# Optimization experiments

Measured on AMD Instinct MI355X. Metric: run time of the kernel, lower is better.

The kernel has to match this reference:

```python
import jax, jax.numpy as jnp
import numpy as np

C = 256
NUM_HEADS = 8
HEAD_DIM = C // NUM_HEADS
SCALE = HEAD_DIM ** -0.5


def setup_inputs() -> dict:
    key = jax.random.key(0)
    ks = jax.random.split(key, 10)
    B, H, W = 2, 64, 64
    s = 0.02
    return {
        "spatial_feat": jax.random.normal(ks[0], (B, C, H, W), jnp.float32),
        "freq_feat": jax.random.normal(ks[1], (B, C, H, W), jnp.float32),
        "wq": jax.random.normal(ks[2], (C, C), jnp.float32) * s,
        "bq": jax.random.normal(ks[3], (C,), jnp.float32) * s,
        "wk": jax.random.normal(ks[4], (C, C), jnp.float32) * s,
        "bk": jax.random.normal(ks[5], (C,), jnp.float32) * s,
        "wv": jax.random.normal(ks[6], (C, C), jnp.float32) * s,
        "bv": jax.random.normal(ks[7], (C,), jnp.float32) * s,
        "wo": jax.random.normal(ks[8], (C, C), jnp.float32) * s,
        "bo": jax.random.normal(ks[9], (C,), jnp.float32) * s,
    }


def _proj(x, w, b):
    # 1x1 conv == channel-mixing matmul: (O,C) x (B,C,H,W) -> (B,O,H,W)
    return jnp.einsum('oc,bchw->bohw', w, x) + b[None, :, None, None]


def _heads(x, B, HW):
    return x.reshape(B, NUM_HEADS, HEAD_DIM, HW)


def _cross_attend(q_src, kv_src, wq, bq, wk, bk, wv, bv, wo, bo):
    B, Cc, H, W = q_src.shape
    HW = H * W
    q = _heads(_proj(q_src, wq, bq), B, HW)   # (B, h, d, N)
    k = _heads(_proj(kv_src, wk, bk), B, HW)
    v = _heads(_proj(kv_src, wv, bv), B, HW)
    # attn[b,h,m,n] = q[...,m] . k[...,n]
    attn = jnp.einsum('bhdm,bhdn->bhmn', q, k) * SCALE
    attn = jax.nn.softmax(attn, axis=-1)
    # out[...,m] = sum_n v[...,n] * attn[m,n]
    out = jnp.einsum('bhdn,bhmn->bhdm', v, attn)
    out = out.reshape(B, Cc, H, W)
    return _proj(out, wo, bo)


def reference(spatial_feat, freq_feat, wq, bq, wk, bk, wv, bv, wo, bo):
    spatial_attended = spatial_feat + _cross_attend(
        spatial_feat, freq_feat, wq, bq, wk, bk, wv, bv, wo, bo)
    freq_attended = freq_feat + _cross_attend(
        freq_feat, spatial_feat, wq, bq, wk, bk, wv, bv, wo, bo)
    return spatial_attended + freq_attended
```

## Files before the change

### kernel.cpp

```cpp
#include <hip/hip_runtime.h>
#include <hip/hip_bf16.h>

#define B_ 2
#define C_ 256
#define NH_ 8
#define D_ 32
#define N_ 4096
#define SCALE_ 0.17677669529663689f
#define QSC_ 0.25505277f

typedef __hip_bfloat16 bf16;
typedef __attribute__((ext_vector_type(8))) short sx8;
typedef __attribute__((ext_vector_type(4))) short sx4;
typedef __attribute__((ext_vector_type(4))) float fx4;

__device__ __forceinline__ float b2f(bf16 x) { return __bfloat162float(x); }
__device__ __forceinline__ bf16 f2b(float x) { return __float2bfloat16(x); }
__device__ __forceinline__ short fbs(float x) { bf16 h = __float2bfloat16(x); return *(short*)&h; }
__device__ __forceinline__ float sbf(short s) { bf16 h = *(bf16*)&s; return __bfloat162float(h); }
__device__ __forceinline__ void sched_mem_fence() { asm volatile("" ::: "memory"); }

#if __has_builtin(__builtin_amdgcn_exp2f)
__device__ __forceinline__ float fexp2(float x) { return __builtin_amdgcn_exp2f(x); }
#else
__device__ __forceinline__ float fexp2(float x) { return exp2f(x); }
#endif

__global__ __launch_bounds__(256)
void convert_x_kernel(const float* __restrict__ spatial,
                      const float* __restrict__ freq,
                      bf16* __restrict__ xb) {
  const int tid = threadIdx.x;
  const int p0 = blockIdx.x * 64;
  const int c0 = blockIdx.y * 64;
  const int z  = blockIdx.z;
  const int s = z >> 1, b = z & 1;
  const float* x = (s == 0) ? spatial : freq;

  __shared__ float ls[64][65];

  const int pp = tid & 63, cb = tid >> 6;
  #pragma unroll
  for (int i = 0; i < 16; ++i) {
    int c = cb + 4 * i;
    ls[c][pp] = x[(size_t)(b * C_ + c0 + c) * N_ + p0 + pp];
  }
  __syncthreads();

  #pragma unroll
  for (int i = 0; i < 2; ++i) {
    int j = tid + 256 * i;
    int p = j >> 3, ck = (j & 7) * 8;
    short tmp[8];
    #pragma unroll
    for (int u = 0; u < 8; ++u) tmp[u] = fbs(ls[ck + u][p]);
    *(sx8*)(xb + ((size_t)z * N_ + p0 + p) * C_ + c0 + ck) = *(sx8*)tmp;
  }
}

__global__ __launch_bounds__(256)
void convert_w_kernel(const float* __restrict__ wq, const float* __restrict__ wk,
                      const float* __restrict__ wv, const float* __restrict__ wo,
                      bf16* __restrict__ wb, bf16* __restrict__ wob) {
  int idx = blockIdx.x * 256 + threadIdx.x;
  if (idx < 196608) {
    const float* src = (idx < 65536) ? wq : (idx < 131072) ? wk : wv;
    wb[idx] = f2b(src[idx & 65535]);
  } else {
    int off = idx - 196608;
    wob[off] = f2b(wo[off]);
  }
}

__global__ __launch_bounds__(256)
void qkv_gemm_kernel(const bf16* __restrict__ wb, const bf16* __restrict__ xb,
                     const float* __restrict__ bq, const float* __restrict__ bk,
                     const float* __restrict__ bv,
                     bf16* __restrict__ qhf, bf16* __restrict__ khf,
                     bf16* __restrict__ vhf) {
  const int tid = threadIdx.x;
  const int p0 = blockIdx.x * 128;
  const int o0 = blockIdx.y * 128;
  const int z  = blockIdx.z;

  const int lane = tid & 63, w = tid >> 6;
  const int ml = lane & 15, Q4 = (lane >> 4) * 4, Q8 = (lane >> 4) * 8;
  const int ow = (w >> 1) * 64, pw = (w & 1) * 64;

  __shared__ __align__(16) short asb[128 * 72];
  __shared__ __align__(16) short bsb[128 * 72];
  __shared__ float bias_s[128];

  if (tid < 128) {
    int o = o0 + tid;
    bias_s[tid] = (o < 256) ? bq[o] : (o < 512) ? bk[o - 256] : bv[o - 512];
  }

  const fx4 z4 = {0.f, 0.f, 0.f, 0.f};
  fx4 acc[4][4];
  #pragma unroll
  for (int ot = 0; ot < 4; ++ot)
    #pragma unroll
    for (int pt = 0; pt < 4; ++pt) acc[ot][pt] = z4;

  const int sr = tid >> 1, scu = (tid & 1) * 32;
  for (int k0 = 0; k0 < 256; k0 += 64) {
    __syncthreads();
    #pragma unroll
    for (int u = 0; u < 4; ++u) {
      *(sx8*)&asb[sr * 72 + scu + u * 8] =
          *(const sx8*)&wb[(o0 + sr) * 256 + k0 + scu + u * 8];
      *(sx8*)&bsb[sr * 72 + scu + u * 8] =
          *(const sx8*)(xb + ((size_t)z * N_ + p0 + sr) * C_ + k0 + scu + u * 8);
    }
    __syncthreads();
    #pragma unroll
    for (int kk = 0; kk < 2; ++kk) {
      sx8 af[4], bfr[4];
      #pragma unroll
      for (int t = 0; t < 4; ++t)
        af[t] = *(sx8*)&asb[(ow + t * 16 + ml) * 72 + kk * 32 + Q8];
      #pragma unroll
      for (int t = 0; t < 4; ++t)
        bfr[t] = *(sx8*)&bsb[(pw + t * 16 + ml) * 72 + kk * 32 + Q8];
      #pragma unroll
      for (int ot = 0; ot < 4; ++ot)
        #pragma unroll
        for (int pt = 0; pt < 4; ++pt)
          acc[ot][pt] = __builtin_amdgcn_mfma_f32_16x16x32_bf16(
              af[ot], bfr[pt], acc[ot][pt], 0, 0, 0);
    }
  }

  if (o0 < 512) {
    bf16* dst = (o0 < 256) ? qhf : khf;
    const int ob = (o0 < 256) ? o0 : o0 - 256;
    const float scl = (o0 < 256) ? QSC_ : 1.f;
    #pragma unroll
    for (int ot = 0; ot < 4; ++ot) {
      const int og = ob + ow + ot * 16 + Q4;
      #pragma unroll
      for (int pt = 0; pt < 4; ++pt) {
        int p = p0 + pw + pt * 16 + ml;
        short tmp[4];
        #pragma unroll
        for (int r = 0; r < 4; ++r)
          tmp[r] = fbs((acc[ot][pt][r] + bias_s[ow + ot * 16 + Q4 + r]) * scl);
        *(sx4*)(dst + (((size_t)z * NH_ + (og >> 5)) * N_ + p) * D_ + (og & 31)) =
            *(sx4*)tmp;
      }
    }
  } else {
    #pragma unroll
    for (int ot = 0; ot < 4; ++ot)
      #pragma unroll
      for (int pt = 0; pt < 4; ++pt) {
        int p = p0 + pw + pt * 16 + ml;
        #pragma unroll
        for (int r = 0; r < 4; ++r) {
          int lo = ow + ot * 16 + Q4 + r;
          int rho = (o0 - 512) + lo;
          int h = rho >> 5, d = rho & 31;
          size_t basev = ((size_t)z * NH_ + h) * D_ * N_;
          vhf[basev + (size_t)(((p >> 5) * 2) + (d >> 4)) * 512 +
              (d & 15) * 32 + (p & 31)] = f2b(acc[ot][pt][r] + bias_s[lo]);
        }
      }
  }
}

__global__ __launch_bounds__(256, 4)
void attn_kernel(const bf16* __restrict__ qhf, const bf16* __restrict__ khf,
                 const bf16* __restrict__ vhf, bf16* __restrict__ attoT) {
  const int tid  = threadIdx.x;
  const int m0   = blockIdx.x * 256;
  const int h    = blockIdx.y;
  const int z    = blockIdx.z;
  const int s = z >> 1, b = z & 1;
  const int zo = ((1 - s) << 1) | b;

  const bf16* qz = qhf + ((size_t)z  * NH_ + h) * N_ * D_;
  const bf16* kz = khf + ((size_t)zo * NH_ + h) * N_ * D_;
  const bf16* vz = vhf + ((size_t)zo * NH_ + h) * D_ * N_;

  const int lane = tid & 63;
  const int w    = tid >> 6;
  const int ml   = lane & 15;
  const int Q4   = (lane >> 4) * 4;
  const int Q8   = (lane >> 4) * 8;

  __shared__ __align__(16) short kts[2][64 * 40];
  __shared__ __align__(16) short vss[2][4][16 * 36];
  __shared__ __align__(16) short pst[4][16 * 72];

  sx8 qf[4];
  #pragma unroll
  for (int s4 = 0; s4 < 4; ++s4)
    qf[s4] = *(const sx8*)(qz + (size_t)(m0 + w * 64 + s4 * 16 + ml) * D_ + Q8);

  sx8 onesf;
  #pragma unroll
  for (int u = 0; u < 8; ++u) onesf[u] = (short)0x3F80;

  const fx4 z4 = {0.f, 0.f, 0.f, 0.f};
  fx4 acc[4][2];
  #pragma unroll
  for (int s4 = 0; s4 < 4; ++s4) { acc[s4][0] = z4; acc[s4][1] = z4; }
  fx4 lacc[4] = {z4, z4, z4, z4};

  const int srow = tid >> 2, sg = (tid & 3) * 8;
  const int vblk = tid >> 6, vrow = (tid >> 2) & 15;

  sx8 kpre = *(const sx8*)(kz + (size_t)tid * 8);
  sx8 vpre = *(const sx8*)(vz + (size_t)tid * 8);
  *(sx8*)&kts[0][srow * 40 + sg] = kpre;
  *(sx8*)&vss[0][vblk][vrow * 36 + sg] = vpre;
  __syncthreads();

  int cur = 0;
  for (int n0 = 0; n0 < N_; n0 += 64) {
    const bool more = (n0 + 64 < N_);
    if (more) {
      kpre = *(const sx8*)(kz + (size_t)(n0 + 64) * D_ + (size_t)tid * 8);
      vpre = *(const sx8*)(vz + (size_t)(n0 + 64) * D_ + (size_t)tid * 8);
    }

    sx8 kf[4], vf[2][2];
    #pragma unroll
    for (int t = 0; t < 4; ++t)
      kf[t] = *(sx8*)&kts[cur][(t * 16 + ml) * 40 + Q8];
    #pragma unroll
    for (int dt = 0; dt < 2; ++dt)
      #pragma unroll
      for (int c = 0; c < 2; ++c)
        vf[dt][c] = *(sx8*)&vss[cur][c * 2 + dt][ml * 36 + Q8];

    #pragma unroll
    for (int s4 = 0; s4 < 4; ++s4) {
      fx4 st[4];
      #pragma unroll
      for (int t = 0; t < 4; ++t)
        st[t] = __builtin_amdgcn_mfma_f32_16x16x32_bf16(kf[t], qf[s4], z4, 0, 0, 0);
      #pragma unroll
      for (int t = 0; t < 4; ++t) {
        #pragma unroll
        for (int r = 0; r < 4; ++r) st[t][r] = fexp2(st[t][r]);
        sx4 pk = {fbs(st[t][0]), fbs(st[t][1]), fbs(st[t][2]), fbs(st[t][3])};
        *(sx4*)&pst[w][ml * 72 + t * 16 + Q4] = pk;
      }
      sched_mem_fence();
      sx8 pf0 = *(sx8*)&pst[w][ml * 72 + 0  + Q8];
      sx8 pf1 = *(sx8*)&pst[w][ml * 72 + 32 + Q8];
      sched_mem_fence();
      lacc[s4] = __builtin_amdgcn_mfma_f32_16x16x32_bf16(onesf, pf0, lacc[s4], 0, 0, 0);
      lacc[s4] = __builtin_amdgcn_mfma_f32_16x16x32_bf16(onesf, pf1, lacc[s4], 0, 0, 0);
      #pragma unroll
      for (int dt = 0; dt < 2; ++dt) {
        fx4 a = acc[s4][dt];
        a = __builtin_amdgcn_mfma_f32_16x16x32_bf16(vf[dt][0], pf0, a, 0, 0, 0);
        a = __builtin_amdgcn_mfma_f32_16x16x32_bf16(vf[dt][1], pf1, a, 0, 0, 0);
        acc[s4][dt] = a;
      }
    }

    if (more) {
      *(sx8*)&kts[cur ^ 1][srow * 40 + sg] = kpre;
      *(sx8*)&vss[cur ^ 1][vblk][vrow * 36 + sg] = vpre;
    }
    __syncthreads();
    cur ^= 1;
  }

  #pragma unroll
  for (int s4 = 0; s4 < 4; ++s4) {
    float inv = 1.f / lacc[s4][0];
    int col = m0 + w * 64 + s4 * 16 + ml;
    #pragma unroll
    for (int dt = 0; dt < 2; ++dt) {
      short tmp[4];
      #pragma unroll
      for (int r = 0; r < 4; ++r) tmp[r] = fbs(acc[s4][dt][r] * inv);
      *(sx4*)(attoT + ((size_t)z * N_ + col) * C_ + h * D_ + dt * 16 + Q4) =
          *(sx4*)tmp;
    }
  }
}

__global__ __launch_bounds__(256)
void out_proj_kernel(const bf16* __restrict__ wob, const bf16* __restrict__ attoT,
                     const float* __restrict__ spatial,
                     const float* __restrict__ freq,
                     const float* __restrict__ bo, float* __restrict__ out) {
  const int tid = threadIdx.x;
  const int p0 = blockIdx.x * 128;
  const int o0 = blockIdx.y * 64;
  const int b  = blockIdx.z;

  const int lane = tid & 63, w = tid >> 6;
  const int ml = lane & 15, Q4 = (lane >> 4) * 4, Q8 = (lane >> 4) * 8;
  const int ow = (w >> 1) * 32, pw = (w & 1) * 64;

  __shared__ __align__(16) short asb[64 * 72];
  __shared__ __align__(16) short bsb[128 * 72];
  __shared__ float bo_s[64];

  if (tid < 64) bo_s[tid] = 2.f * bo[o0 + tid];

  const bf16* at0 = attoT + (size_t)(0 + b) * N_ * C_;
  const bf16* at1 = attoT + (size_t)(2 + b) * N_ * C_;

  const fx4 z4 = {0.f, 0.f, 0.f, 0.f};
  fx4 acc[2][4];
  #pragma unroll
  for (int ot = 0; ot < 2; ++ot)
    #pragma unroll
    for (int pt = 0; pt < 4; ++pt) acc[ot][pt] = z4;

  for (int k0 = 0; k0 < 256; k0 += 64) {
    __syncthreads();
    #pragma unroll
    for (int i = 0; i < 2; ++i) {
      int j = tid + 256 * i;
      int r = j >> 3, cu = (j & 7) * 8;
      *(sx8*)&asb[r * 72 + cu] = *(const sx8*)&wob[(o0 + r) * 256 + k0 + cu];
    }
    #pragma unroll
    for (int i = 0; i < 4; ++i) {
      int j = tid + 256 * i;
      int p = j >> 3, cu = (j & 7) * 8;
      sx8 va = *(const sx8*)(at0 + (size_t)(p0 + p) * C_ + k0 + cu);
      sx8 vb2 = *(const sx8*)(at1 + (size_t)(p0 + p) * C_ + k0 + cu);
      short tmp[8];
      #pragma unroll
      for (int u = 0; u < 8; ++u) tmp[u] = fbs(sbf(va[u]) + sbf(vb2[u]));
      *(sx8*)&bsb[p * 72 + cu] = *(sx8*)tmp;
    }
    __syncthreads();
    #pragma unroll
    for (int kk = 0; kk < 2; ++kk) {
      sx8 af[2], bfr[4];
      #pragma unroll
      for (int t = 0; t < 2; ++t)
        af[t] = *(sx8*)&asb[(ow + t * 16 + ml) * 72 + kk * 32 + Q8];
      #pragma unroll
      for (int t = 0; t < 4; ++t)
        bfr[t] = *(sx8*)&bsb[(pw + t * 16 + ml) * 72 + kk * 32 + Q8];
      #pragma unroll
      for (int ot = 0; ot < 2; ++ot)
        #pragma unroll
        for (int pt = 0; pt < 4; ++pt)
          acc[ot][pt] = __builtin_amdgcn_mfma_f32_16x16x32_bf16(
              af[ot], bfr[pt], acc[ot][pt], 0, 0, 0);
    }
  }

  #pragma unroll
  for (int ot = 0; ot < 2; ++ot)
    #pragma unroll
    for (int pt = 0; pt < 4; ++pt) {
      int p = p0 + pw + pt * 16 + ml;
      #pragma unroll
      for (int r = 0; r < 4; ++r) {
        int ol = ow + ot * 16 + Q4 + r;
        size_t off = ((size_t)b * C_ + o0 + ol) * N_ + p;
        out[off] = acc[ot][pt][r] + bo_s[ol] + spatial[off] + freq[off];
      }
    }
}

extern "C" void kernel_launch(void* const* d_in, const int* in_sizes, int n_in,
                              void* d_out, int out_size, void* d_ws, size_t ws_size,
                              hipStream_t stream) {
  const float* spatial = (const float*)d_in[0];
  const float* freq    = (const float*)d_in[1];
  const float* wq = (const float*)d_in[2];
  const float* bq = (const float*)d_in[3];
  const float* wk = (const float*)d_in[4];
  const float* bk = (const float*)d_in[5];
  const float* wv = (const float*)d_in[6];
  const float* bv = (const float*)d_in[7];
  const float* wo = (const float*)d_in[8];
  const float* bo = (const float*)d_in[9];
  float* out = (float*)d_out;

  const size_t SZ = (size_t)2 * B_ * N_ * C_;
  bf16* xb    = (bf16*)d_ws;
  bf16* qhf   = xb + SZ;
  bf16* khf   = qhf + SZ;
  bf16* vhf   = khf + SZ;
  bf16* attoT = vhf + SZ;
  bf16* wb    = attoT + SZ;
  bf16* wob   = wb + 768 * 256;

  convert_w_kernel<<<dim3(1024), 256, 0, stream>>>(wq, wk, wv, wo, wb, wob);
  convert_x_kernel<<<dim3(N_ / 64, C_ / 64, 2 * B_), 256, 0, stream>>>(
      spatial, freq, xb);
  qkv_gemm_kernel<<<dim3(N_ / 128, 768 / 128, 2 * B_), 256, 0, stream>>>(
      wb, xb, bq, bk, bv, qhf, khf, vhf);
  attn_kernel<<<dim3(N_ / 256, NH_, 2 * B_), 256, 0, stream>>>(
      qhf, khf, vhf, attoT);
  out_proj_kernel<<<dim3(N_ / 128, C_ / 64, B_), 256, 0, stream>>>(
      wob, attoT, spatial, freq, bo, out);
}
```

Baseline: 227.3 us.

## Split attention KV range in two with combine kernel and swizzle LDS layouts

Attention blocks now each process half of the key/value sequence, doubling the grid so more blocks run concurrently on the GPU. Unnormalised partial outputs and row sums are written to workspace, and a new combine kernel adds them and normalises. K and P shared-memory tiles switch from padded strides to XOR swizzles to cut bank conflicts and LDS footprint. The cost is an extra kernel launch and extra global traffic for the partials, and the split path is used only if the workspace is large enough.

```diff
diff --git a/kernel.cpp b/kernel.cpp
--- a/kernel.cpp
+++ b/kernel.cpp
@@ -169,13 +169,17 @@
   }
 }
 
+template<int NSPLIT>
 __global__ __launch_bounds__(256, 4)
-void attn_kernel(const bf16* __restrict__ qhf, const bf16* __restrict__ khf,
-                 const bf16* __restrict__ vhf, bf16* __restrict__ attoT) {
+void attn_kernel_t(const bf16* __restrict__ qhf, const bf16* __restrict__ khf,
+                   const bf16* __restrict__ vhf, bf16* __restrict__ outp,
+                   float* __restrict__ lpart) {
   const int tid  = threadIdx.x;
   const int m0   = blockIdx.x * 256;
   const int h    = blockIdx.y;
-  const int z    = blockIdx.z;
+  const int bz   = blockIdx.z;
+  const int sp   = (NSPLIT == 1) ? 0 : (bz >> 2);
+  const int z    = (NSPLIT == 1) ? bz : (bz & 3);
   const int s = z >> 1, b = z & 1;
   const int zo = ((1 - s) << 1) | b;
 
@@ -186,12 +190,16 @@
   const int lane = tid & 63;
   const int w    = tid >> 6;
   const int ml   = lane & 15;
-  const int Q4   = (lane >> 4) * 4;
-  const int Q8   = (lane >> 4) * 8;
-
-  __shared__ __align__(16) short kts[2][64 * 40];
+  const int q4   = lane >> 4;
+  const int Q4   = q4 * 4;
+  const int Q8   = q4 * 8;
+
+  __shared__ __align__(16) short kts[2][64 * 32];
   __shared__ __align__(16) short vss[2][4][16 * 36];
-  __shared__ __align__(16) short pst[4][16 * 72];
+  __shared__ __align__(16) short pst[4][16 * 64];
+
+  const int nlo = sp * (N_ / NSPLIT);
+  const int nhi = nlo + N_ / NSPLIT;
 
   sx8 qf[4];
   #pragma unroll
@@ -208,18 +216,23 @@
   for (int s4 = 0; s4 < 4; ++s4) { acc[s4][0] = z4; acc[s4][1] = z4; }
   fx4 lacc[4] = {z4, z4, z4, z4};
 
-  const int srow = tid >> 2, sg = (tid & 3) * 8;
-  const int vblk = tid >> 6, vrow = (tid >> 2) & 15;
-
-  sx8 kpre = *(const sx8*)(kz + (size_t)tid * 8);
-  sx8 vpre = *(const sx8*)(vz + (size_t)tid * 8);
-  *(sx8*)&kts[0][srow * 40 + sg] = kpre;
-  *(sx8*)&vss[0][vblk][vrow * 36 + sg] = vpre;
+  const int srow = tid >> 2;
+  const int ksw  = ((tid & 3) ^ (srow & 3)) * 8;
+  const int vblk = tid >> 6, vrow = (tid >> 2) & 15, vg = (tid & 3) * 8;
+  const int kfg  = (q4 ^ (ml & 3)) * 8;
+  const int psw  = ml & 7;
+  const int pr0  = ml * 64 + ((q4 ^ psw) * 8);
+  const int pr1  = ml * 64 + (((4 + q4) ^ psw) * 8);
+
+  sx8 kpre = *(const sx8*)(kz + (size_t)nlo * D_ + (size_t)tid * 8);
+  sx8 vpre = *(const sx8*)(vz + (size_t)nlo * D_ + (size_t)tid * 8);
+  *(sx8*)&kts[0][srow * 32 + ksw] = kpre;
+  *(sx8*)&vss[0][vblk][vrow * 36 + vg] = vpre;
   __syncthreads();
 
   int cur = 0;
-  for (int n0 = 0; n0 < N_; n0 += 64) {
-    const bool more = (n0 + 64 < N_);
+  for (int n0 = nlo; n0 < nhi; n0 += 64) {
+    const bool more = (n0 + 64 < nhi);
     if (more) {
       kpre = *(const sx8*)(kz + (size_t)(n0 + 64) * D_ + (size_t)tid * 8);
       vpre = *(const sx8*)(vz + (size_t)(n0 + 64) * D_ + (size_t)tid * 8);
@@ -228,7 +241,7 @@
     sx8 kf[4], vf[2][2];
     #pragma unroll
     for (int t = 0; t < 4; ++t)
-      kf[t] = *(sx8*)&kts[cur][(t * 16 + ml) * 40 + Q8];
+      kf[t] = *(sx8*)&kts[cur][(t * 16 + ml) * 32 + kfg];
     #pragma unroll
     for (int dt = 0; dt < 2; ++dt)
       #pragma unroll
@@ -246,11 +259,12 @@
         #pragma unroll
         for (int r = 0; r < 4; ++r) st[t][r] = fexp2(st[t][r]);
         sx4 pk = {fbs(st[t][0]), fbs(st[t][1]), fbs(st[t][2]), fbs(st[t][3])};
-        *(sx4*)&pst[w][ml * 72 + t * 16 + Q4] = pk;
+        *(sx4*)&pst[w][ml * 64 + (((2 * t + (q4 >> 1)) ^ psw) * 8) +
+                       4 * (q4 & 1)] = pk;
       }
       sched_mem_fence();
-      sx8 pf0 = *(sx8*)&pst[w][ml * 72 + 0  + Q8];
-      sx8 pf1 = *(sx8*)&pst[w][ml * 72 + 32 + Q8];
+      sx8 pf0 = *(sx8*)&pst[w][pr0];
+      sx8 pf1 = *(sx8*)&pst[w][pr1];
       sched_mem_fence();
       lacc[s4] = __builtin_amdgcn_mfma_f32_16x16x32_bf16(onesf, pf0, lacc[s4], 0, 0, 0);
       lacc[s4] = __builtin_amdgcn_mfma_f32_16x16x32_bf16(onesf, pf1, lacc[s4], 0, 0, 0);
@@ -264,8 +278,8 @@
     }
 
     if (more) {
-      *(sx8*)&kts[cur ^ 1][srow * 40 + sg] = kpre;
-      *(sx8*)&vss[cur ^ 1][vblk][vrow * 36 + sg] = vpre;
+      *(sx8*)&kts[cur ^ 1][srow * 32 + ksw] = kpre;
+      *(sx8*)&vss[cur ^ 1][vblk][vrow * 36 + vg] = vpre;
     }
     __syncthreads();
     cur ^= 1;
@@ -273,17 +287,53 @@
 
   #pragma unroll
   for (int s4 = 0; s4 < 4; ++s4) {
-    float inv = 1.f / lacc[s4][0];
     int col = m0 + w * 64 + s4 * 16 + ml;
-    #pragma unroll
-    for (int dt = 0; dt < 2; ++dt) {
-      short tmp[4];
-      #pragma unroll
-      for (int r = 0; r < 4; ++r) tmp[r] = fbs(acc[s4][dt][r] * inv);
-      *(sx4*)(attoT + ((size_t)z * N_ + col) * C_ + h * D_ + dt * 16 + Q4) =
-          *(sx4*)tmp;
-    }
-  }
+    if (NSPLIT == 1) {
+      float inv = 1.f / lacc[s4][0];
+      #pragma unroll
+      for (int dt = 0; dt < 2; ++dt) {
+        short tmp[4];
+        #pragma unroll
+        for (int r = 0; r < 4; ++r) tmp[r] = fbs(acc[s4][dt][r] * inv);
+        *(sx4*)(outp + ((size_t)z * N_ + col) * C_ + h * D_ + dt * 16 + Q4) =
+            *(sx4*)tmp;
+      }
+    } else {
+      size_t ob = (((size_t)(sp * 4 + z) * NH_ + h) * N_ + col) * D_;
+      #pragma unroll
+      for (int dt = 0; dt < 2; ++dt) {
+        short tmp[4];
+        #pragma unroll
+        for (int r = 0; r < 4; ++r) tmp[r] = fbs(acc[s4][dt][r]);
+        *(sx4*)(outp + ob + dt * 16 + Q4) = *(sx4*)tmp;
+      }
+      if (q4 == 0)
+        lpart[((size_t)(sp * 4 + z) * NH_ + h) * N_ + col] = lacc[s4][0];
+    }
+  }
+}
+
+__global__ __launch_bounds__(256)
+void combine_kernel(const bf16* __restrict__ opart,
+                    const float* __restrict__ lpart,
+                    bf16* __restrict__ attoT) {
+  int flat = blockIdx.x * 256 + threadIdx.x;
+  int g = flat & 31;
+  int n = (flat >> 5) & (N_ - 1);
+  int z = flat >> 17;
+  int h = g >> 2, d0 = (g & 3) * 8;
+
+  size_t i0 = (((size_t)(0 + z) * NH_ + h) * N_ + n) * D_ + d0;
+  size_t i1 = (((size_t)(4 + z) * NH_ + h) * N_ + n) * D_ + d0;
+  sx8 a = *(const sx8*)(opart + i0);
+  sx8 c = *(const sx8*)(opart + i1);
+  float l = lpart[((size_t)(0 + z) * NH_ + h) * N_ + n] +
+            lpart[((size_t)(4 + z) * NH_ + h) * N_ + n];
+  float inv = 1.f / l;
+  short tmp[8];
+  #pragma unroll
+  for (int u = 0; u < 8; ++u) tmp[u] = fbs((sbf(a[u]) + sbf(c[u])) * inv);
+  *(sx8*)(attoT + ((size_t)z * N_ + n) * C_ + g * 8) = *(sx8*)tmp;
 }
 
 __global__ __launch_bounds__(256)
@@ -391,14 +441,26 @@
   bf16* attoT = vhf + SZ;
   bf16* wb    = attoT + SZ;
   bf16* wob   = wb + 768 * 256;
+  bf16* opart = wob + 256 * 256;
+  const size_t OP = (size_t)2 * 4 * NH_ * N_ * D_;
+  float* lpart = (float*)(opart + OP);
+  const size_t LP = (size_t)2 * 4 * NH_ * N_;
+  size_t need2 = (size_t)((char*)(lpart + LP) - (char*)d_ws);
+  const bool split2 = (ws_size >= need2);
 
   convert_w_kernel<<<dim3(1024), 256, 0, stream>>>(wq, wk, wv, wo, wb, wob);
   convert_x_kernel<<<dim3(N_ / 64, C_ / 64, 2 * B_), 256, 0, stream>>>(
       spatial, freq, xb);
   qkv_gemm_kernel<<<dim3(N_ / 128, 768 / 128, 2 * B_), 256, 0, stream>>>(
       wb, xb, bq, bk, bv, qhf, khf, vhf);
-  attn_kernel<<<dim3(N_ / 256, NH_, 2 * B_), 256, 0, stream>>>(
-      qhf, khf, vhf, attoT);
+  if (split2) {
+    attn_kernel_t<2><<<dim3(N_ / 256, NH_, 8), 256, 0, stream>>>(
+        qhf, khf, vhf, opart, lpart);
+    combine_kernel<<<dim3(2048), 256, 0, stream>>>(opart, lpart, attoT);
+  } else {
+    attn_kernel_t<1><<<dim3(N_ / 256, NH_, 4), 256, 0, stream>>>(
+        qhf, khf, vhf, attoT, nullptr);
+  }
   out_proj_kernel<<<dim3(N_ / 128, C_ / 64, B_), 256, 0, stream>>>(
       wob, attoT, spatial, freq, bo, out);
 }
```

Result: no change. 231.5 us (+1.8%).
